# Kernel optimization log

Hardware: AMD Instinct MI355X
Metric: run time of the kernel (lower is better)

The kernel has to match this reference:

```python
import jax, jax.numpy as jnp
import numpy as np

N_KERNELS = 11

def _kernel_mus(n):
    l = [1.0]
    bs = 2.0 / (n - 1)
    l.append(1 - bs / 2)
    for i in range(1, n - 1):
        l.append(l[i] - bs)
    return l

def _kernel_sigmas(n):
    bs = 2.0 / (n - 1)
    return [0.001] + [0.5 * bs] * (n - 1)

MU = jnp.asarray(_kernel_mus(N_KERNELS), jnp.float32)      # [K]
SIGMA = jnp.asarray(_kernel_sigmas(N_KERNELS), jnp.float32)  # [K]


def setup_inputs() -> dict:
    key = jax.random.key(0)
    ks = jax.random.split(key, 10)
    V, E, C = 50000, 300, 128
    B, Q, D = 128, 30, 200
    inp = {
        'query_tokens': jax.random.randint(ks[0], (B, Q), 0, V),
        'document_tokens': jax.random.randint(ks[1], (B, D), 0, V),
        'embedding': jax.random.normal(ks[2], (V, E), jnp.float32) * 0.1,
        'conv_w1': jax.random.normal(ks[3], (C, E, 1), jnp.float32) * 0.05,
        'conv_w2': jax.random.normal(ks[4], (C, E, 2), jnp.float32) * 0.05,
        'conv_w3': jax.random.normal(ks[5], (C, E, 3), jnp.float32) * 0.05,
        'conv_b1': jax.random.normal(ks[6], (C,), jnp.float32) * 0.01,
        'conv_b2': jax.random.normal(ks[7], (C,), jnp.float32) * 0.01,
        'conv_b3': jax.random.normal(ks[8], (C,), jnp.float32) * 0.01,
        'dense_w': jax.random.uniform(ks[9], (1, N_KERNELS * 9), jnp.float32, -0.014, 0.014),
    }
    return inp


def _conv_ngram(x_ble, w, b):
    # x_ble: [B, L, E]; w: [C, E, k]; pad (0, k-1) on the length dim -> same length out
    x = x_ble.transpose(0, 2, 1)  # [B, E, L]
    y = jax.lax.conv_general_dilated(
        x, w, window_strides=(1,), padding=[(0, w.shape[2] - 1)],
        dimension_numbers=('NCH', 'OIH', 'NCH'))
    return jax.nn.relu(y + b[None, :, None]).transpose(0, 2, 1)  # [B, L, C]


def _kernel_pool(q, d, qd_mask, q_mask):
    # q: [B,Q,C], d: [B,D,C]; cosine sim -> Gaussian RBF soft-binning -> masked log-sum pooling
    qn = q / (jnp.linalg.norm(q, axis=-1, keepdims=True) + 1e-13)
    dn = d / (jnp.linalg.norm(d, axis=-1, keepdims=True) + 1e-13)
    cos = jnp.einsum('bqc,bdc->bqd', qn, dn) * qd_mask           # [B,Q,D]
    diff = cos[..., None] - MU                                    # [B,Q,D,K]
    kern = jnp.exp(-(diff * diff) / (2.0 * SIGMA * SIGMA)) * qd_mask[..., None]
    per_kernel_query = jnp.sum(kern, axis=2)                      # [B,Q,K]
    logk = jnp.log(jnp.clip(per_kernel_query, 1e-10)) * 0.01
    return jnp.sum(logk * q_mask[..., None], axis=1)              # [B,K]


def reference(query_tokens, document_tokens, embedding,
              conv_w1, conv_w2, conv_w3, conv_b1, conv_b2, conv_b3, dense_w):
    q_mask = (query_tokens > 0).astype(jnp.float32)               # [B,Q]
    d_mask = (document_tokens > 0).astype(jnp.float32)            # [B,D]
    qd_mask = q_mask[:, :, None] * d_mask[:, None, :]             # [B,Q,D]

    q_emb = embedding[query_tokens]                               # [B,Q,E]
    d_emb = embedding[document_tokens]                            # [B,D,E]

    convs = [(conv_w1, conv_b1), (conv_w2, conv_b2), (conv_w3, conv_b3)]
    q_grams = [_conv_ngram(q_emb, w, b) for w, b in convs]
    d_grams = [_conv_ngram(d_emb, w, b) for w, b in convs]

    feats = jnp.concatenate(
        [_kernel_pool(q, d, qd_mask, q_mask) for q in q_grams for d in d_grams],
        axis=1)                                                   # [B, K*9]
    return (feats @ dense_w.T)[:, 0]                              # [B]
```

## Files before the change

### kernel.cpp

```cpp
#include <hip/hip_runtime.h>
#include <hip/hip_bf16.h>
#include <math.h>

#define B_   128
#define Qn   30
#define Dn   200
#define En   300

typedef __attribute__((ext_vector_type(8))) short short8;
typedef __attribute__((ext_vector_type(4))) float floatx4;
typedef unsigned int u32;
typedef unsigned short u16;

static __device__ __forceinline__ u16 f2b(float x) {
    union { float f; u32 u; } v; v.f = x;
    u32 r = v.u + 0x7FFFu + ((v.u >> 16) & 1u);
    return (u16)(r >> 16);
}
static __device__ __forceinline__ float bits2f(u32 u) {
    union { u32 u2; float f; } v; v.u2 = u; return v.f;
}

__global__ void prep_kernel(
    const float* __restrict__ w1, const float* __restrict__ w2, const float* __restrict__ w3,
    u16* __restrict__ Wt3)
{
    int p = (blockIdx.x*128 + blockIdx.y)*256 + threadIdx.x;
    if (p >= 245760) return;
    int ks = p / 24576;
    int r  = p - ks*24576;
    int g, rr;
    if (r < 4096)        { g = 0; rr = r;         }
    else if (r < 12288)  { g = 1; rr = r - 4096;  }
    else                 { g = 2; rr = r - 12288; }
    int j  = rr >> 12;
    int r2 = rr & 4095;
    int nt  = r2 >> 9;
    int q4  = (r2 >> 7) & 3;
    int c16 = (r2 >> 3) & 15;
    int k8  = r2 & 7;
    int ch = nt*16 + c16;
    int e  = ks*32 + q4*8 + k8;
    float v = 0.f;
    if (e < En) {
        if (g == 0)      v = w1[ch*En + e];
        else if (g == 1) v = w2[(ch*En + e)*2 + j];
        else             v = w3[(ch*En + e)*3 + j];
    }
    Wt3[p] = f2b(v);
}

__global__ __launch_bounds__(512, 4) void conv_kernel(
    const int* __restrict__ qtok, const int* __restrict__ dtok,
    const float* __restrict__ emb,
    const u16* __restrict__ Wt3,
    const float* __restrict__ b1, const float* __restrict__ b2, const float* __restrict__ b3,
    u16* __restrict__ qg, u16* __restrict__ dg,
    float* __restrict__ invnq, float* __restrict__ invnd)
{
    __shared__ __align__(16) char smem[43560];
    char* As  = smem;
    int*  toks = (int*)(smem + 43296);

    const int tile = blockIdx.x;
    const int tid = threadIdx.x;
    const int wv = tid >> 6, lane = tid & 63;
    const int l15 = lane & 15, qd4 = lane >> 4;
    const int mh = wv >> 2, nh = wv & 3;
    const int gR0 = tile*64;

    if (tid < 66) {
        int gr = gR0 + tid;
        int t = -1;
        if (gr < 32768) {
            int b = gr >> 8, pos = gr & 255;
            if (pos < Dn) t = dtok[b*Dn + pos];
            else if (pos >= 208 && pos < 238) t = qtok[b*Qn + (pos - 208)];
        }
        toks[tid] = t;
    }
    __syncthreads();

    #pragma unroll
    for (int i = 0; i < 11; ++i) {
        int idx = tid + i*512;
        if (idx < 5280) {
            int r = idx / 80, c4 = idx - r*80;
            int t = toks[r];
            u16 o0=0,o1=0,o2=0,o3=0;
            if (t >= 0 && c4 < 75) {
                float4 v = *(const float4*)(emb + t*En + c4*4);
                o0=f2b(v.x); o1=f2b(v.y); o2=f2b(v.z); o3=f2b(v.w);
            }
            u16* pdst = (u16*)(As + r*656 + c4*8);
            pdst[0]=o0; pdst[1]=o1; pdst[2]=o2; pdst[3]=o3;
        }
    }

    float bias[3][2];
    #pragma unroll
    for (int nt = 0; nt < 2; ++nt) {
        int ch = nh*32 + nt*16 + l15;
        bias[0][nt] = b1[ch];
        bias[1][nt] = b2[ch];
        bias[2][nt] = b3[ch];
    }

    floatx4 acc[3][2][2];
    #pragma unroll
    for (int g = 0; g < 3; ++g)
        #pragma unroll
        for (int mt = 0; mt < 2; ++mt)
            #pragma unroll
            for (int nt = 0; nt < 2; ++nt)
                acc[g][mt][nt] = (floatx4){0.f,0.f,0.f,0.f};

    __syncthreads();

    #pragma unroll 1
    for (int ks = 0; ks < 10; ++ks) {
        short8 af[2][3];
        #pragma unroll
        for (int mt = 0; mt < 2; ++mt)
            #pragma unroll
            for (int j = 0; j < 3; ++j)
                af[mt][j] = *(const short8*)(As + (mh*32 + mt*16 + l15 + j)*656 + ks*64 + qd4*16);
        const u16* Wks = Wt3 + ks*24576;
        #pragma unroll
        for (int g = 0; g < 3; ++g) {
            const int cbW = (g == 0) ? 0 : (g == 1) ? 4096 : 12288;
            #pragma unroll
            for (int j = 0; j <= g; ++j) {
                const u16* bb = Wks + cbW + (j*8 + nh*2)*512 + lane*8;
                short8 w0  = *(const short8*)(bb);
                short8 w1v = *(const short8*)(bb + 512);
                #pragma unroll
                for (int mt = 0; mt < 2; ++mt) {
                    acc[g][mt][0] = __builtin_amdgcn_mfma_f32_16x16x32_bf16(
                        af[mt][j], w0,  acc[g][mt][0], 0, 0, 0);
                    acc[g][mt][1] = __builtin_amdgcn_mfma_f32_16x16x32_bf16(
                        af[mt][j], w1v, acc[g][mt][1], 0, 0, 0);
                }
            }
        }
    }

    u16* Gs = (u16*)smem;
    #pragma unroll
    for (int g = 0; g < 3; ++g) {
        __syncthreads();
        #pragma unroll
        for (int mt = 0; mt < 2; ++mt)
            #pragma unroll
            for (int nt = 0; nt < 2; ++nt) {
                int ch = nh*32 + nt*16 + l15;
                #pragma unroll
                for (int i = 0; i < 4; ++i) {
                    int row = mh*32 + mt*16 + qd4*4 + i;
                    Gs[row*136 + ch] = f2b(fmaxf(acc[g][mt][nt][i] + bias[g][nt], 0.f));
                }
            }
        __syncthreads();

        if (tid < 64) {
            const char* rp = (const char*)Gs + tid*272;
            float ssum = 0.f;
            #pragma unroll
            for (int t16 = 0; t16 < 16; ++t16) {
                uint4 u = *(const uint4*)(rp + t16*16);
                float x;
                x = bits2f(u.x << 16); ssum += x*x;  x = bits2f(u.x & 0xffff0000u); ssum += x*x;
                x = bits2f(u.y << 16); ssum += x*x;  x = bits2f(u.y & 0xffff0000u); ssum += x*x;
                x = bits2f(u.z << 16); ssum += x*x;  x = bits2f(u.z & 0xffff0000u); ssum += x*x;
                x = bits2f(u.w << 16); ssum += x*x;  x = bits2f(u.w & 0xffff0000u); ssum += x*x;
            }
            float inv = 1.f / (sqrtf(ssum) + 1e-13f);
            int gr = gR0 + tid;
            int b = gr >> 8, pos = gr & 255;
            if (pos < 208)      invnd[(g*B_ + b)*208 + pos] = inv;
            else if (pos < 238) invnq[(g*B_ + b)*32 + (pos - 208)] = inv;
        }
        #pragma unroll
        for (int i = 0; i < 2; ++i) {
            int idx = tid + i*512;
            int r = idx >> 4, c16 = idx & 15;
            uint4 v = *(const uint4*)((const char*)Gs + r*272 + c16*16);
            int gr = gR0 + r;
            int b = gr >> 8, pos = gr & 255;
            if (pos < 208)      *(uint4*)(dg + ((g*B_ + b)*208 + pos)*128 + c16*8) = v;
            else if (pos < 238) *(uint4*)(qg + ((g*B_ + b)*32 + (pos - 208))*128 + c16*8) = v;
        }
    }
}

__global__ __launch_bounds__(256, 2) void pool_kernel(
    const u16* __restrict__ qg, const u16* __restrict__ dg,
    const float* __restrict__ invnq, const float* __restrict__ invnd,
    const int* __restrict__ qtok, const int* __restrict__ dtok,
    float* __restrict__ feats)
{
    __shared__ __align__(16) u16 dsb[208*136];
    __shared__ float pk[96*12];
    __shared__ float invqA[96];
    __shared__ float qmA[96];
    __shared__ __align__(16) float invd[208];

    const int tid = threadIdx.x;
    const int b = blockIdx.y, dj = blockIdx.x;
    const int wv = tid >> 6, lane = tid & 63;
    const int l15 = lane & 15, qd4 = lane >> 4;

    for (int idx = tid; idx < 208*16; idx += 256) {
        int r = idx >> 4, ch = idx & 15;
        uint4 v = make_uint4(0u,0u,0u,0u);
        if (r < Dn) v = *(const uint4*)(dg + ((dj*B_ + b)*208 + r)*128 + ch*8);
        *(uint4*)((char*)dsb + r*272 + ch*16) = v;
    }
    if (tid < 208) {
        float v = invnd[(dj*B_ + b)*208 + tid];
        bool ok = (tid < Dn) && (dtok[b*Dn + tid] > 0);
        invd[tid] = ok ? v : (-fabsf(v) - 1.0f);
    }
    if (tid < 96) {
        int qi = tid >> 5, qr = tid & 31;
        float v = invnq[(qi*B_ + b)*32 + qr];
        bool ok = (qr < Qn) && (qtok[b*Qn + qr] > 0);
        invqA[tid] = ok ? v : 0.f;
        qmA[tid] = ok ? 1.f : 0.f;
    }
    for (int i = tid; i < 96*12; i += 256) pk[i] = 0.f;
    __syncthreads();

    const float CkR[9] = {8886110.5f, 162754.79f, 2980.958f, 54.598150f, 1.0f,
                          0.018315639f, 3.3546263e-4f, 6.1442124e-6f, 1.1253517e-7f};

    for (int qi = 0; qi < 3; ++qi) {
        short8 qf[2][4];
        float vq[2];
        #pragma unroll
        for (int qt = 0; qt < 2; ++qt) {
            vq[qt] = invqA[qi*32 + qt*16 + l15];
            #pragma unroll
            for (int ks = 0; ks < 4; ++ks)
                qf[qt][ks] = *(const short8*)(qg + ((qi*B_ + b)*32 + qt*16 + l15)*128 + ks*32 + qd4*8);
        }
        float pkl[2][11];
        #pragma unroll
        for (int qt = 0; qt < 2; ++qt)
            #pragma unroll
            for (int k = 0; k < 11; ++k) pkl[qt][k] = 0.f;

        for (int t = wv; t < 13; t += 4) {
            short8 af[4];
            #pragma unroll
            for (int ks = 0; ks < 4; ++ks)
                af[ks] = *(const short8*)((const char*)dsb + (t*16 + l15)*272 + ks*64 + qd4*16);
            floatx4 acc[2];
            acc[0] = (floatx4){0.f,0.f,0.f,0.f};
            acc[1] = (floatx4){0.f,0.f,0.f,0.f};
            #pragma unroll
            for (int ks = 0; ks < 4; ++ks)
                #pragma unroll
                for (int qt = 0; qt < 2; ++qt)
                    acc[qt] = __builtin_amdgcn_mfma_f32_16x16x32_bf16(af[ks], qf[qt][ks], acc[qt], 0, 0, 0);
            floatx4 iv4 = *(const floatx4*)(invd + t*16 + qd4*4);
            #pragma unroll
            for (int qt = 0; qt < 2; ++qt)
                #pragma unroll
                for (int i = 0; i < 4; ++i) {
                    float cs = acc[qt][i] * vq[qt] * iv4[i];
                    cs = (cs > 0.f) ? cs : 2.0f;
                    float t0 = cs - 1.0f;
                    float u  = cs - 0.9f;
                    float s0 = __expf(-500000.f * t0 * t0);
                    float e  = __expf(-50.f * u * u);
                    float rr = __expf(-20.f * cs);
                    pkl[qt][0] += s0;
                    pkl[qt][1] += e;
                    #pragma unroll
                    for (int kk = 0; kk < 9; ++kk) {
                        e = e * rr * CkR[kk];
                        pkl[qt][2 + kk] += e;
                    }
                }
        }
        #pragma unroll
        for (int qt = 0; qt < 2; ++qt)
            #pragma unroll
            for (int k = 0; k < 11; ++k) {
                float v = pkl[qt][k];
                v += __shfl_xor(v, 16);
                v += __shfl_xor(v, 32);
                if (qd4 == 0) atomicAdd(&pk[(qi*32 + qt*16 + l15)*12 + k], v);
            }
    }
    __syncthreads();

    if (tid < 33) {
        int qi = tid / 11, k = tid - qi*11;
        float s = 0.f;
        for (int q = 0; q < Qn; ++q)
            s += qmA[qi*32 + q] * 0.01f * __logf(fmaxf(pk[(qi*32 + q)*12 + k], 1e-10f));
        feats[(b*9 + qi*3 + dj)*11 + k] = s;
    }
}

__global__ void final_kernel(const float* __restrict__ feats,
                             const float* __restrict__ dw,
                             float* __restrict__ out) {
    int b = threadIdx.x;
    if (b < B_) {
        float s = 0.f;
        for (int f = 0; f < 99; ++f) s += feats[b*99 + f] * dw[f];
        out[b] = s;
    }
}

extern "C" void kernel_launch(void* const* d_in, const int* in_sizes, int n_in,
                              void* d_out, int out_size, void* d_ws, size_t ws_size,
                              hipStream_t stream) {
    const int*   qtok = (const int*)d_in[0];
    const int*   dtok = (const int*)d_in[1];
    const float* emb  = (const float*)d_in[2];
    const float* w1   = (const float*)d_in[3];
    const float* w2   = (const float*)d_in[4];
    const float* w3   = (const float*)d_in[5];
    const float* b1   = (const float*)d_in[6];
    const float* b2   = (const float*)d_in[7];
    const float* b3   = (const float*)d_in[8];
    const float* dw   = (const float*)d_in[9];
    float* out = (float*)d_out;

    char* w = (char*)d_ws;
    u16*   Wt3   = (u16*)w;
    u16*   qg    = (u16*)(w + 491520);
    u16*   dgm   = (u16*)(w + 3637248);
    float* invq_ = (float*)(w + 24084480);
    float* invd_ = (float*)(w + 24133632);
    float* feats = (float*)(w + 24453120);

    prep_kernel<<<dim3(8, B_), 256, 0, stream>>>(w1, w2, w3, Wt3);

    conv_kernel<<<dim3(512), 512, 0, stream>>>(
        qtok, dtok, emb, Wt3, b1, b2, b3, qg, dgm, invq_, invd_);

    pool_kernel<<<dim3(3, B_), 256, 0, stream>>>(qg, dgm, invq_, invd_, qtok, dtok, feats);

    final_kernel<<<1, 128, 0, stream>>>(feats, dw, out);
}
```

Baseline: 166.3 us.

## Split conv embedding staging into halves and widen pool kernel to one wave per tile

The conv kernel now stages only the first half of the embedding columns into shared memory, issues the global loads for the second half into registers, and runs the first five K-steps before converting and storing the rest, so the gather latency overlaps MFMA work. The row-norm computation is spread across all 512 threads with shuffle reductions instead of 64 threads each looping over a full row. The pool kernel is launched with 1024 threads so each of the 13 document tiles gets its own wave, holding its A fragments and inverse norms once across the three query grams. The cost is more registers held in the conv kernel for the prefetched data, and a higher thread count per block in the pool kernel, with 3 of its 16 waves idle.

```diff
diff --git a/kernel.cpp b/kernel.cpp
--- a/kernel.cpp
+++ b/kernel.cpp
@@ -82,13 +82,13 @@
     __syncthreads();
 
     #pragma unroll
-    for (int i = 0; i < 11; ++i) {
+    for (int i = 0; i < 6; ++i) {
         int idx = tid + i*512;
-        if (idx < 5280) {
-            int r = idx / 80, c4 = idx - r*80;
+        if (idx < 2640) {
+            int r = idx / 40, c4 = idx - r*40;
             int t = toks[r];
             u16 o0=0,o1=0,o2=0,o3=0;
-            if (t >= 0 && c4 < 75) {
+            if (t >= 0) {
                 float4 v = *(const float4*)(emb + t*En + c4*4);
                 o0=f2b(v.x); o1=f2b(v.y); o2=f2b(v.z); o3=f2b(v.w);
             }
@@ -117,8 +117,21 @@
 
     __syncthreads();
 
+    float4 hf[6];
+    #pragma unroll
+    for (int i = 0; i < 6; ++i) {
+        int idx = tid + i*512;
+        const float* p = emb;
+        if (idx < 2640) {
+            int r = idx / 40, c = idx - r*40;
+            int t = toks[r];
+            if (t >= 0 && c < 35) p = emb + t*En + (40 + c)*4;
+        }
+        hf[i] = *(const float4*)p;
+    }
+
     #pragma unroll 1
-    for (int ks = 0; ks < 10; ++ks) {
+    for (int ks = 0; ks < 5; ++ks) {
         short8 af[2][3];
         #pragma unroll
         for (int mt = 0; mt < 2; ++mt)
@@ -145,6 +158,49 @@
         }
     }
 
+    #pragma unroll
+    for (int i = 0; i < 6; ++i) {
+        int idx = tid + i*512;
+        if (idx < 2640) {
+            int r = idx / 40, c = idx - r*40;
+            int t = toks[r];
+            bool ok = (t >= 0) && (c < 35);
+            u16 o0=0,o1=0,o2=0,o3=0;
+            if (ok) { o0=f2b(hf[i].x); o1=f2b(hf[i].y); o2=f2b(hf[i].z); o3=f2b(hf[i].w); }
+            u16* pdst = (u16*)(As + r*656 + (40 + c)*8);
+            pdst[0]=o0; pdst[1]=o1; pdst[2]=o2; pdst[3]=o3;
+        }
+    }
+    __syncthreads();
+
+    #pragma unroll 1
+    for (int ks = 5; ks < 10; ++ks) {
+        short8 af[2][3];
+        #pragma unroll
+        for (int mt = 0; mt < 2; ++mt)
+            #pragma unroll
+            for (int j = 0; j < 3; ++j)
+                af[mt][j] = *(const short8*)(As + (mh*32 + mt*16 + l15 + j)*656 + ks*64 + qd4*16);
+        const u16* Wks = Wt3 + ks*24576;
+        #pragma unroll
+        for (int g = 0; g < 3; ++g) {
+            const int cbW = (g == 0) ? 0 : (g == 1) ? 4096 : 12288;
+            #pragma unroll
+            for (int j = 0; j <= g; ++j) {
+                const u16* bb = Wks + cbW + (j*8 + nh*2)*512 + lane*8;
+                short8 w0  = *(const short8*)(bb);
+                short8 w1v = *(const short8*)(bb + 512);
+                #pragma unroll
+                for (int mt = 0; mt < 2; ++mt) {
+                    acc[g][mt][0] = __builtin_amdgcn_mfma_f32_16x16x32_bf16(
+                        af[mt][j], w0,  acc[g][mt][0], 0, 0, 0);
+                    acc[g][mt][1] = __builtin_amdgcn_mfma_f32_16x16x32_bf16(
+                        af[mt][j], w1v, acc[g][mt][1], 0, 0, 0);
+                }
+            }
+        }
+    }
+
     u16* Gs = (u16*)smem;
     #pragma unroll
     for (int g = 0; g < 3; ++g) {
@@ -162,23 +218,29 @@
             }
         __syncthreads();
 
-        if (tid < 64) {
-            const char* rp = (const char*)Gs + tid*272;
+        {
+            int r = tid >> 3, pp = tid & 7;
+            const char* rp = (const char*)Gs + r*272 + pp*32;
             float ssum = 0.f;
             #pragma unroll
-            for (int t16 = 0; t16 < 16; ++t16) {
-                uint4 u = *(const uint4*)(rp + t16*16);
+            for (int t2 = 0; t2 < 2; ++t2) {
+                uint4 u = *(const uint4*)(rp + t2*16);
                 float x;
                 x = bits2f(u.x << 16); ssum += x*x;  x = bits2f(u.x & 0xffff0000u); ssum += x*x;
                 x = bits2f(u.y << 16); ssum += x*x;  x = bits2f(u.y & 0xffff0000u); ssum += x*x;
                 x = bits2f(u.z << 16); ssum += x*x;  x = bits2f(u.z & 0xffff0000u); ssum += x*x;
                 x = bits2f(u.w << 16); ssum += x*x;  x = bits2f(u.w & 0xffff0000u); ssum += x*x;
             }
-            float inv = 1.f / (sqrtf(ssum) + 1e-13f);
-            int gr = gR0 + tid;
-            int b = gr >> 8, pos = gr & 255;
-            if (pos < 208)      invnd[(g*B_ + b)*208 + pos] = inv;
-            else if (pos < 238) invnq[(g*B_ + b)*32 + (pos - 208)] = inv;
+            ssum += __shfl_xor(ssum, 1);
+            ssum += __shfl_xor(ssum, 2);
+            ssum += __shfl_xor(ssum, 4);
+            if (pp == 0) {
+                float inv = 1.f / (sqrtf(ssum) + 1e-13f);
+                int gr = gR0 + r;
+                int b = gr >> 8, pos = gr & 255;
+                if (pos < 208)      invnd[(g*B_ + b)*208 + pos] = inv;
+                else if (pos < 238) invnq[(g*B_ + b)*32 + (pos - 208)] = inv;
+            }
         }
         #pragma unroll
         for (int i = 0; i < 2; ++i) {
@@ -193,7 +255,7 @@
     }
 }
 
-__global__ __launch_bounds__(256, 2) void pool_kernel(
+__global__ __launch_bounds__(1024, 2) void pool_kernel(
     const u16* __restrict__ qg, const u16* __restrict__ dg,
     const float* __restrict__ invnq, const float* __restrict__ invnd,
     const int* __restrict__ qtok, const int* __restrict__ dtok,
@@ -210,7 +272,7 @@
     const int wv = tid >> 6, lane = tid & 63;
     const int l15 = lane & 15, qd4 = lane >> 4;
 
-    for (int idx = tid; idx < 208*16; idx += 256) {
+    for (int idx = tid; idx < 208*16; idx += 1024) {
         int r = idx >> 4, ch = idx & 15;
         uint4 v = make_uint4(0u,0u,0u,0u);
         if (r < Dn) v = *(const uint4*)(dg + ((dj*B_ + b)*208 + r)*128 + ch*8);
@@ -228,33 +290,31 @@
         invqA[tid] = ok ? v : 0.f;
         qmA[tid] = ok ? 1.f : 0.f;
     }
-    for (int i = tid; i < 96*12; i += 256) pk[i] = 0.f;
+    for (int i = tid; i < 96*12; i += 1024) pk[i] = 0.f;
     __syncthreads();
 
     const float CkR[9] = {8886110.5f, 162754.79f, 2980.958f, 54.598150f, 1.0f,
                           0.018315639f, 3.3546263e-4f, 6.1442124e-6f, 1.1253517e-7f};
 
-    for (int qi = 0; qi < 3; ++qi) {
-        short8 qf[2][4];
-        float vq[2];
-        #pragma unroll
-        for (int qt = 0; qt < 2; ++qt) {
-            vq[qt] = invqA[qi*32 + qt*16 + l15];
-            #pragma unroll
-            for (int ks = 0; ks < 4; ++ks)
-                qf[qt][ks] = *(const short8*)(qg + ((qi*B_ + b)*32 + qt*16 + l15)*128 + ks*32 + qd4*8);
-        }
-        float pkl[2][11];
-        #pragma unroll
-        for (int qt = 0; qt < 2; ++qt)
-            #pragma unroll
-            for (int k = 0; k < 11; ++k) pkl[qt][k] = 0.f;
-
-        for (int t = wv; t < 13; t += 4) {
-            short8 af[4];
-            #pragma unroll
-            for (int ks = 0; ks < 4; ++ks)
-                af[ks] = *(const short8*)((const char*)dsb + (t*16 + l15)*272 + ks*64 + qd4*16);
+    if (wv < 13) {
+        const int t = wv;
+        short8 af[4];
+        #pragma unroll
+        for (int ks = 0; ks < 4; ++ks)
+            af[ks] = *(const short8*)((const char*)dsb + (t*16 + l15)*272 + ks*64 + qd4*16);
+        floatx4 iv4 = *(const floatx4*)(invd + t*16 + qd4*4);
+
+        #pragma unroll 1
+        for (int qi = 0; qi < 3; ++qi) {
+            short8 qf[2][4];
+            float vq[2];
+            #pragma unroll
+            for (int qt = 0; qt < 2; ++qt) {
+                vq[qt] = invqA[qi*32 + qt*16 + l15];
+                #pragma unroll
+                for (int ks = 0; ks < 4; ++ks)
+                    qf[qt][ks] = *(const short8*)(qg + ((qi*B_ + b)*32 + qt*16 + l15)*128 + ks*32 + qd4*8);
+            }
             floatx4 acc[2];
             acc[0] = (floatx4){0.f,0.f,0.f,0.f};
             acc[1] = (floatx4){0.f,0.f,0.f,0.f};
@@ -263,7 +323,13 @@
                 #pragma unroll
                 for (int qt = 0; qt < 2; ++qt)
                     acc[qt] = __builtin_amdgcn_mfma_f32_16x16x32_bf16(af[ks], qf[qt][ks], acc[qt], 0, 0, 0);
-            floatx4 iv4 = *(const floatx4*)(invd + t*16 + qd4*4);
+
+            float pkl[2][11];
+            #pragma unroll
+            for (int qt = 0; qt < 2; ++qt)
+                #pragma unroll
+                for (int k = 0; k < 11; ++k) pkl[qt][k] = 0.f;
+
             #pragma unroll
             for (int qt = 0; qt < 2; ++qt)
                 #pragma unroll
@@ -283,16 +349,16 @@
                         pkl[qt][2 + kk] += e;
                     }
                 }
-        }
-        #pragma unroll
-        for (int qt = 0; qt < 2; ++qt)
-            #pragma unroll
-            for (int k = 0; k < 11; ++k) {
-                float v = pkl[qt][k];
-                v += __shfl_xor(v, 16);
-                v += __shfl_xor(v, 32);
-                if (qd4 == 0) atomicAdd(&pk[(qi*32 + qt*16 + l15)*12 + k], v);
-            }
+            #pragma unroll
+            for (int qt = 0; qt < 2; ++qt)
+                #pragma unroll
+                for (int k = 0; k < 11; ++k) {
+                    float v = pkl[qt][k];
+                    v += __shfl_xor(v, 16);
+                    v += __shfl_xor(v, 32);
+                    if (qd4 == 0) atomicAdd(&pk[(qi*32 + qt*16 + l15)*12 + k], v);
+                }
+        }
     }
     __syncthreads();
 
@@ -344,7 +410,7 @@
     conv_kernel<<<dim3(512), 512, 0, stream>>>(
         qtok, dtok, emb, Wt3, b1, b2, b3, qg, dgm, invq_, invd_);
 
-    pool_kernel<<<dim3(3, B_), 256, 0, stream>>>(qg, dgm, invq_, invd_, qtok, dtok, feats);
+    pool_kernel<<<dim3(3, B_), 1024, 0, stream>>>(qg, dgm, invq_, invd_, qtok, dtok, feats);
 
     final_kernel<<<1, 128, 0, stream>>>(feats, dw, out);
 }
```

Result: slower. 189.9 us (+14.2%).
